# Optimization experiments

Measured on AMD Instinct MI355X. Metric: run time of the kernel, lower is better.

## Reference

```python
import jax, jax.numpy as jnp
import numpy as np

T, H, P = 8192, 512, 512
DT_MIN, DT_MAX = 0.001, 0.1
STEP_RESCALE = 1.0


def setup_inputs() -> dict:
    key = jax.random.key(0)
    ks = jax.random.split(key, 8)
    x = jax.random.normal(ks[0], (T, H), dtype=jnp.float32)
    # sparse reset flags (episode boundaries)
    mask = jax.random.bernoulli(ks[1], 0.005, (T,)).astype(jnp.float32)
    carry = jnp.zeros((1, P, 2), dtype=jnp.float32)  # initial complex state as (re, im)
    # HiPPO-DPLR-style eigenvalue init: lambda_k = -0.5 + i*pi*k
    lambda_real = -0.5 * jnp.ones((P,), dtype=jnp.float32)
    lambda_imag = jnp.pi * jnp.arange(P, dtype=jnp.float32)
    b = jax.random.normal(ks[2], (P, H, 2), dtype=jnp.float32) / np.sqrt(H)
    c = jax.random.normal(ks[3], (H, P, 2), dtype=jnp.float32) * np.sqrt(0.5)
    d = jax.random.normal(ks[4], (H,), dtype=jnp.float32)
    u = jax.random.uniform(ks[5], (P, 1), dtype=jnp.float32)
    log_step = np.log(DT_MIN) + u * (np.log(DT_MAX) - np.log(DT_MIN))
    return {"x": x, "mask": mask, "carry": carry, "lambda_real": lambda_real,
            "lambda_imag": lambda_imag, "b": b, "c": c, "d": d, "log_step": log_step}


def _binary_operator_reset(q_i, q_j):
    a_i, b_i, c_i = q_i
    a_j, b_j, c_j = q_j
    a_out = a_j * a_i * (1.0 - c_j) + a_j * c_j
    b_out = (a_j * b_i + b_j) * (1.0 - c_j) + b_j * c_j
    c_out = c_i * (1.0 - c_j) + c_j
    return (a_out, b_out, c_out)


def reference(x, mask, carry, lambda_real, lambda_imag, b, c, d, log_step):
    t = x.shape[0]
    # clip_eigens=True: force stability
    lam_re = jnp.minimum(lambda_real, -0.0001)
    lam = jax.lax.complex(lam_re, lambda_imag).astype(jnp.complex64)  # [P]
    b_tilde = jax.lax.complex(b[..., 0], b[..., 1]).astype(jnp.complex64)  # [P,H]
    c_tilde = jax.lax.complex(c[..., 0], c[..., 1]).astype(jnp.complex64)  # [H,P]
    step = (STEP_RESCALE * jnp.exp(log_step[:, 0].astype(jnp.float32))).astype(jnp.complex64)  # [P]
    # ZOH discretization
    lambda_bar = jnp.exp(lam * step)                      # [P]
    b_bar = ((lambda_bar - 1.0) / lam)[:, None] * b_tilde  # [P,H]
    # scan elements
    a = jnp.broadcast_to(lambda_bar, (t, P))
    a = jnp.concatenate([jnp.ones((1, P), dtype=lambda_bar.dtype), a])  # [T+1,P]
    b_x = x.astype(jnp.complex64) @ b_bar.T                              # [T,P]
    carry0 = jax.lax.complex(carry[..., 0], carry[..., 1]).astype(jnp.complex64)  # [1,P]
    b_x = jnp.concatenate([carry0, b_x])                                 # [T+1,P]
    m = jnp.concatenate([jnp.zeros((1,), x.dtype), mask])[:, None]       # [T+1,1]
    _, states, _ = jax.lax.associative_scan(_binary_operator_reset, (a, b_x, m))
    states = states[1:]                                                  # [T,P] complex
    ys = jnp.real(states @ c_tilde.T) + d * x                            # [T,H]
    final_carry = states[-1][None]                                       # [1,P] complex
    return (final_carry, ys)
```

## Files before the change

### kernel.cpp

```cpp
#include <hip/hip_runtime.h>
#include <hip/hip_bf16.h>

#define T_LEN 8192
#define H_DIM 512
#define P_DIM 512
#define CS 16
#define NB (T_LEN / CS)

typedef __attribute__((ext_vector_type(8))) __bf16 bf16x8;
typedef __attribute__((ext_vector_type(4))) float f32x4;

__device__ __forceinline__ unsigned short f2bf(float f) {
    __bf16 h = (__bf16)f;
    return __builtin_bit_cast(unsigned short, h);
}
__device__ __forceinline__ float bf2f(unsigned short u) {
    unsigned v = ((unsigned)u) << 16;
    return __builtin_bit_cast(float, v);
}

__device__ __forceinline__ void gload_lds16(void* g, void* l) {
    __builtin_amdgcn_global_load_lds(
        (__attribute__((address_space(1))) unsigned*)g,
        (__attribute__((address_space(3))) unsigned*)l, 16, 0, 0);
}

__global__ __launch_bounds__(512) void precompute_p1(
    const float* __restrict__ lambda_real,
    const float* __restrict__ lambda_imag,
    const float* __restrict__ log_step,
    double* __restrict__ lbar,
    double* __restrict__ coef) {
    int p = threadIdx.x;
    double lr = fmin((double)lambda_real[p], -1e-4);
    double li = (double)lambda_imag[p];
    double step = exp((double)log_step[p]);
    double er = exp(lr * step);
    double ang = li * step;
    double lbr = er * cos(ang);
    double lbi = er * sin(ang);
    lbar[2 * p] = lbr;
    lbar[2 * p + 1] = lbi;
    double nr = lbr - 1.0, ni = lbi;
    double den = lr * lr + li * li;
    coef[2 * p]     = (nr * lr + ni * li) / den;
    coef[2 * p + 1] = (ni * lr - nr * li) / den;
}

__global__ __launch_bounds__(256) void prep_kernel(
    const float* __restrict__ x,
    const float* __restrict__ b, const float* __restrict__ c,
    const double* __restrict__ coef,
    unsigned short* __restrict__ xhi, unsigned short* __restrict__ xlo,
    unsigned short* __restrict__ Bt1hi, unsigned short* __restrict__ Bt1lo,
    unsigned short* __restrict__ Bt2hi, unsigned short* __restrict__ Bt2lo) {
    int idx = blockIdx.x * 256 + threadIdx.x;
    {
        float4 v = ((const float4*)x)[idx];
        ushort4 h, l;
        h.x = f2bf(v.x); l.x = f2bf(v.x - bf2f(h.x));
        h.y = f2bf(v.y); l.y = f2bf(v.y - bf2f(h.y));
        h.z = f2bf(v.z); l.z = f2bf(v.z - bf2f(h.z));
        h.w = f2bf(v.w); l.w = f2bf(v.w - bf2f(h.w));
        ((ushort4*)xhi)[idx] = h;
        ((ushort4*)xlo)[idx] = l;
    }
    if (blockIdx.x < (P_DIM * H_DIM) / 256) {
        int idx2 = blockIdx.x * 256 + threadIdx.x;
        {
            int p = idx2 >> 9, h = idx2 & 511;
            double cr = coef[2 * p], ci = coef[2 * p + 1];
            float2 bv = ((const float2*)b)[(size_t)p * H_DIM + h];
            float re = (float)(cr * (double)bv.x - ci * (double)bv.y);
            float im = (float)(cr * (double)bv.y + ci * (double)bv.x);
            unsigned short rh = f2bf(re), ih = f2bf(im);
            Bt1hi[(size_t)(2 * p) * H_DIM + h]     = rh;
            Bt1lo[(size_t)(2 * p) * H_DIM + h]     = f2bf(re - bf2f(rh));
            Bt1hi[(size_t)(2 * p + 1) * H_DIM + h] = ih;
            Bt1lo[(size_t)(2 * p + 1) * H_DIM + h] = f2bf(im - bf2f(ih));
        }
        {
            int h = idx2 >> 9, p = idx2 & 511;
            float2 cv = ((const float2*)c)[(size_t)h * P_DIM + p];
            float re = cv.x, im = -cv.y;
            ushort2 hi, lo;
            hi.x = f2bf(re); lo.x = f2bf(re - bf2f(hi.x));
            hi.y = f2bf(im); lo.y = f2bf(im - bf2f(hi.y));
            ((ushort2*)Bt2hi)[(size_t)h * P_DIM + p] = hi;
            ((ushort2*)Bt2lo)[(size_t)h * P_DIM + p] = lo;
        }
    }
}

template <int MODE>
__global__ __launch_bounds__(256) void gemm_mfma_split(
    const unsigned short* __restrict__ Ahi, const unsigned short* __restrict__ Alo,
    int lda,
    const unsigned short* __restrict__ Bthi, const unsigned short* __restrict__ Btlo,
    int ldb,
    void* __restrict__ Cout0, void* __restrict__ Cout1, int ldc, int K,
    const float* __restrict__ Dvec, const float* __restrict__ X,
    const float* __restrict__ mask, const double* __restrict__ lbar,
    double* __restrict__ cA, double* __restrict__ cS, float* __restrict__ cC) {
    __shared__ __align__(16) unsigned short lds[2][4][128 * 32];
    const int tid = threadIdx.x;
    const int lane = tid & 63, wid = tid >> 6;
    const int wm = wid >> 1, wn = wid & 1;

    const int id = blockIdx.y * gridDim.x + blockIdx.x;
    const int nx = gridDim.x, rpx = gridDim.y >> 3;
    const int xcd = id & 7, j = id >> 3;
    const int by = xcd * rpx + j / nx;
    const int bx = j % nx;
    const int bm = by * 128, bn = bx * 128;

    const unsigned short* ssrc;
    int srow0, sld;
    if (wid == 0)      { ssrc = Ahi;  srow0 = bm; sld = lda; }
    else if (wid == 1) { ssrc = Alo;  srow0 = bm; sld = lda; }
    else if (wid == 2) { ssrc = Bthi; srow0 = bn; sld = ldb; }
    else               { ssrc = Btlo; srow0 = bn; sld = ldb; }

    f32x4 acc[4][4];
#pragma unroll
    for (int i = 0; i < 4; ++i)
#pragma unroll
        for (int j2 = 0; j2 < 4; ++j2) acc[i][j2] = (f32x4)(0.0f);

    auto stage = [&](int buf, int k0) {
        unsigned short* base = &lds[buf][wid][0];
#pragma unroll
        for (int s = 0; s < 8; ++s) {
            int r = s * 16 + (lane >> 2);
            int cg = (lane & 3) ^ ((r >> 1) & 3);
            void* g = (void*)((const char*)(ssrc + (size_t)(srow0 + r) * sld + k0)
                              + cg * 16);
            gload_lds16(g, (void*)((char*)base + s * 1024));
        }
    };

    stage(0, 0);
    __syncthreads();

    const int nk = K / 32;
    for (int t = 0; t < nk; ++t) {
        int cur = t & 1;
        if (t + 1 < nk) stage(cur ^ 1, (t + 1) * 32);

        bf16x8 ah[4], al[4], bh[4], bl[4];
#pragma unroll
        for (int i = 0; i < 4; ++i) {
            int rA = wm * 64 + i * 16 + (lane & 15);
            int byA = rA * 64 + ((((lane >> 4)) ^ ((rA >> 1) & 3)) << 4);
            ah[i] = *(const bf16x8*)((const char*)&lds[cur][0][0] + byA);
            al[i] = *(const bf16x8*)((const char*)&lds[cur][1][0] + byA);
            int rB = wn * 64 + i * 16 + (lane & 15);
            int byB = rB * 64 + ((((lane >> 4)) ^ ((rB >> 1) & 3)) << 4);
            bh[i] = *(const bf16x8*)((const char*)&lds[cur][2][0] + byB);
            bl[i] = *(const bf16x8*)((const char*)&lds[cur][3][0] + byB);
        }
#pragma unroll
        for (int i = 0; i < 4; ++i)
#pragma unroll
            for (int j2 = 0; j2 < 4; ++j2) {
                acc[i][j2] = __builtin_amdgcn_mfma_f32_16x16x32_bf16(
                    ah[i], bh[j2], acc[i][j2], 0, 0, 0);
                acc[i][j2] = __builtin_amdgcn_mfma_f32_16x16x32_bf16(
                    ah[i], bl[j2], acc[i][j2], 0, 0, 0);
                acc[i][j2] = __builtin_amdgcn_mfma_f32_16x16x32_bf16(
                    al[i], bh[j2], acc[i][j2], 0, 0, 0);
            }
        __syncthreads();
    }

#pragma unroll
    for (int i = 0; i < 4; ++i)
#pragma unroll
        for (int j2 = 0; j2 < 4; ++j2) {
            int col = bn + wn * 64 + j2 * 16 + (lane & 15);
#pragma unroll
            for (int r = 0; r < 4; ++r) {
                int row = bm + wm * 64 + i * 16 + (lane >> 4) * 4 + r;
                float v = acc[i][j2][r];
                if (MODE == 0) {
                    unsigned short h = f2bf(v);
                    unsigned short lo = f2bf(v - bf2f(h));
                    ((unsigned short*)Cout0)[(size_t)row * ldc + col] = h;
                    ((unsigned short*)Cout1)[(size_t)row * ldc + col] = lo;
                } else {
                    v += Dvec[col] * X[(size_t)row * ldc + col];
                    ((float*)Cout0)[(size_t)row * ldc + col] = v;
                }
            }
        }

    if constexpr (MODE == 0) {
        float* fl = (float*)&lds[0][0][0];
#pragma unroll
        for (int i = 0; i < 4; ++i)
#pragma unroll
            for (int j2 = 0; j2 < 4; ++j2) {
                int lcol = wn * 64 + j2 * 16 + (lane & 15);
#pragma unroll
                for (int r = 0; r < 4; ++r) {
                    int lrow = wm * 64 + i * 16 + (lane >> 4) * 4 + r;
                    fl[lrow * 128 + lcol] = acc[i][j2][r];
                }
            }
        __syncthreads();
        const int NCH = 128 / CS;
        for (int w = tid; w < 64 * NCH; w += 256) {
            int q = w & 63;
            int ck = w >> 6;
            int pg = (bn >> 1) + q;
            double lbr = lbar[2 * pg], lbi = lbar[2 * pg + 1];
            double Ar = 1., Ai = 0., Sr = 0., Si = 0.;
            float Cc = 0.f;
            for (int k = 0; k < CS; ++k) {
                int row = ck * CS + k;
                float m = mask[bm + row];
                double bxr = (double)fl[row * 128 + 2 * q];
                double bxi = (double)fl[row * 128 + 2 * q + 1];
                if (m != 0.f) {
                    Ar = lbr; Ai = lbi; Sr = bxr; Si = bxi; Cc = 1.f;
                } else {
                    double nAr = lbr * Ar - lbi * Ai;
                    Ai = lbr * Ai + lbi * Ar; Ar = nAr;
                    double nSr = lbr * Sr - lbi * Si + bxr;
                    Si = lbr * Si + lbi * Sr + bxi; Sr = nSr;
                }
            }
            int cg = (bm / CS) + ck;
            cA[(size_t)cg * 1024 + 2 * pg]     = Ar;
            cA[(size_t)cg * 1024 + 2 * pg + 1] = Ai;
            cS[(size_t)cg * 1024 + 2 * pg]     = Sr;
            cS[(size_t)cg * 1024 + 2 * pg + 1] = Si;
            cC[(size_t)cg * P_DIM + pg] = Cc;
        }
    }
}

__global__ __launch_bounds__(NB) void scanB_kernel(
    const double* __restrict__ cA, const double* __restrict__ cS,
    const float* __restrict__ cC, const float* __restrict__ carry,
    double* __restrict__ prefix) {
    int p = blockIdx.x;
    int i = threadIdx.x;
    __shared__ double sAr[NB], sAi[NB], sSr[NB], sSi[NB];
    __shared__ float sC[NB];

    double Ar = cA[(size_t)i * 1024 + 2 * p];
    double Ai = cA[(size_t)i * 1024 + 2 * p + 1];
    double Sr = cS[(size_t)i * 1024 + 2 * p];
    double Si = cS[(size_t)i * 1024 + 2 * p + 1];
    float  C  = cC[(size_t)i * P_DIM + p];
    sAr[i] = Ar; sAi[i] = Ai; sSr[i] = Sr; sSi[i] = Si; sC[i] = C;
    __syncthreads();

    for (int step = 1; step < NB; step <<= 1) {
        double pAr = 0, pAi = 0, pSr = 0, pSi = 0; float pC = 0;
        if (i >= step) {
            pAr = sAr[i - step]; pAi = sAi[i - step];
            pSr = sSr[i - step]; pSi = sSi[i - step]; pC = sC[i - step];
        }
        __syncthreads();
        if (i >= step && C == 0.f) {
            double nAr = Ar * pAr - Ai * pAi;
            double nAi = Ar * pAi + Ai * pAr;
            double nSr = Ar * pSr - Ai * pSi + Sr;
            double nSi = Ar * pSi + Ai * pSr + Si;
            Ar = nAr; Ai = nAi; Sr = nSr; Si = nSi; C = pC;
        }
        sAr[i] = Ar; sAi[i] = Ai; sSr[i] = Sr; sSi[i] = Si; sC[i] = C;
        __syncthreads();
    }

    double c0r = (double)carry[2 * p], c0i = (double)carry[2 * p + 1];
    double pr, pi_;
    if (i == 0) {
        pr = c0r; pi_ = c0i;
    } else {
        double Lr = sAr[i - 1], Li = sAi[i - 1];
        double Tr = sSr[i - 1], Ti = sSi[i - 1];
        float  LC = sC[i - 1];
        if (LC != 0.f) { pr = Tr; pi_ = Ti; }
        else {
            pr  = Lr * c0r - Li * c0i + Tr;
            pi_ = Lr * c0i + Li * c0r + Ti;
        }
    }
    prefix[(size_t)i * 1024 + 2 * p]     = pr;
    prefix[(size_t)i * 1024 + 2 * p + 1] = pi_;
}

__global__ __launch_bounds__(512) void scanC_kernel(
    unsigned short* __restrict__ Shi, unsigned short* __restrict__ Slo,
    const float* __restrict__ mask, const double* __restrict__ lbar,
    const double* __restrict__ prefix,
    float* __restrict__ carry_out, int carry_elems) {
    int p = threadIdx.x;
    int blk = blockIdx.x;
    double lbr = lbar[2 * p], lbi = lbar[2 * p + 1];
    double sr = prefix[(size_t)blk * 1024 + 2 * p];
    double si = prefix[(size_t)blk * 1024 + 2 * p + 1];
    ushort2* H2 = (ushort2*)Shi;
    ushort2* L2 = (ushort2*)Slo;
    int t0 = blk * CS;
    for (int t = t0; t < t0 + CS; ++t) {
        float m = mask[t];
        ushort2 h2 = H2[(size_t)t * P_DIM + p];
        ushort2 l2 = L2[(size_t)t * P_DIM + p];
        double bxr = (double)(bf2f(h2.x) + bf2f(l2.x));
        double bxi = (double)(bf2f(h2.y) + bf2f(l2.y));
        if (m != 0.f) {
            sr = bxr; si = bxi;
        } else {
            double nr = lbr * sr - lbi * si + bxr;
            si = lbr * si + lbi * sr + bxi;
            sr = nr;
        }
        float sf = (float)sr, sif = (float)si;
        ushort2 ho, lo;
        ho.x = f2bf(sf);  lo.x = f2bf(sf - bf2f(ho.x));
        ho.y = f2bf(sif); lo.y = f2bf(sif - bf2f(ho.y));
        H2[(size_t)t * P_DIM + p] = ho;
        L2[(size_t)t * P_DIM + p] = lo;
    }
    if (blk == NB - 1) {
        if (carry_elems >= 1024) {
            carry_out[2 * p] = (float)sr;
            carry_out[2 * p + 1] = (float)si;
        } else {
            carry_out[p] = (float)sr;
        }
    }
}

extern "C" void kernel_launch(void* const* d_in, const int* in_sizes, int n_in,
                              void* d_out, int out_size, void* d_ws, size_t ws_size,
                              hipStream_t stream) {
    const float* x           = (const float*)d_in[0];
    const float* mask        = (const float*)d_in[1];
    const float* carry       = (const float*)d_in[2];
    const float* lambda_real = (const float*)d_in[3];
    const float* lambda_imag = (const float*)d_in[4];
    const float* b           = (const float*)d_in[5];
    const float* c           = (const float*)d_in[6];
    const float* d           = (const float*)d_in[7];
    const float* log_step    = (const float*)d_in[8];

    float* out = (float*)d_out;
    char* ws = (char*)d_ws;

    int carry_elems = out_size - T_LEN * H_DIM;
    if (carry_elems != 512 && carry_elems != 1024) carry_elems = 1024;
    float* ys_out = out + carry_elems;

    double* lbar   = (double*)ws;                        ws += 1024 * 8;
    double* coef   = (double*)ws;                        ws += 1024 * 8;
    double* cA     = (double*)ws;                        ws += (size_t)NB * 1024 * 8;
    double* cSb    = (double*)ws;                        ws += (size_t)NB * 1024 * 8;
    double* prefix = (double*)ws;                        ws += (size_t)NB * 1024 * 8;
    float* cC      = (float*)ws;                         ws += (size_t)NB * P_DIM * 4;
    unsigned short* xhi   = (unsigned short*)ws;         ws += (size_t)T_LEN * H_DIM * 2;
    unsigned short* xlo   = (unsigned short*)ws;         ws += (size_t)T_LEN * H_DIM * 2;
    unsigned short* Bt1hi = (unsigned short*)ws;         ws += (size_t)(2 * P_DIM) * H_DIM * 2;
    unsigned short* Bt1lo = (unsigned short*)ws;         ws += (size_t)(2 * P_DIM) * H_DIM * 2;
    unsigned short* Bt2hi = (unsigned short*)ws;         ws += (size_t)H_DIM * (2 * P_DIM) * 2;
    unsigned short* Bt2lo = (unsigned short*)ws;         ws += (size_t)H_DIM * (2 * P_DIM) * 2;
    unsigned short* Shi   = (unsigned short*)ws;         ws += (size_t)T_LEN * (2 * P_DIM) * 2;
    unsigned short* Slo   = (unsigned short*)ws;         ws += (size_t)T_LEN * (2 * P_DIM) * 2;

    precompute_p1<<<1, 512, 0, stream>>>(lambda_real, lambda_imag, log_step,
                                         lbar, coef);
    prep_kernel<<<(T_LEN * H_DIM / 4) / 256, 256, 0, stream>>>(
        x, b, c, coef, xhi, xlo, Bt1hi, Bt1lo, Bt2hi, Bt2lo);

    {
        dim3 grid((2 * P_DIM) / 128, T_LEN / 128);
        gemm_mfma_split<0><<<grid, 256, 0, stream>>>(
            xhi, xlo, H_DIM, Bt1hi, Bt1lo, H_DIM,
            Shi, Slo, 2 * P_DIM, H_DIM, nullptr, nullptr,
            mask, lbar, cA, cSb, cC);
    }

    scanB_kernel<<<P_DIM, NB, 0, stream>>>(cA, cSb, cC, carry, prefix);
    scanC_kernel<<<NB, 512, 0, stream>>>(Shi, Slo, mask, lbar, prefix, out,
                                         carry_elems);

    {
        dim3 grid(H_DIM / 128, T_LEN / 128);
        gemm_mfma_split<1><<<grid, 256, 0, stream>>>(
            Shi, Slo, 2 * P_DIM, Bt2hi, Bt2lo, 2 * P_DIM,
            ys_out, nullptr, H_DIM, 2 * P_DIM, d, x,
            nullptr, nullptr, nullptr, nullptr, nullptr);
    }
}
```

Before: 111.3 us.

## Drop precompute kernel by recomputing discretization inline; use wave-shuffle scan in scanB

```diff
diff --git a/kernel.cpp b/kernel.cpp
--- a/kernel.cpp
+++ b/kernel.cpp
@@ -25,32 +25,23 @@
         (__attribute__((address_space(3))) unsigned*)l, 16, 0, 0);
 }
 
-__global__ __launch_bounds__(512) void precompute_p1(
-    const float* __restrict__ lambda_real,
-    const float* __restrict__ lambda_imag,
-    const float* __restrict__ log_step,
-    double* __restrict__ lbar,
-    double* __restrict__ coef) {
-    int p = threadIdx.x;
-    double lr = fmin((double)lambda_real[p], -1e-4);
-    double li = (double)lambda_imag[p];
+__device__ __forceinline__ void lbar_of(const float* lam_re, const float* lam_im,
+                                        const float* log_step, int p,
+                                        double& lbr, double& lbi) {
+    double lr = fmin((double)lam_re[p], -1e-4);
+    double li = (double)lam_im[p];
     double step = exp((double)log_step[p]);
     double er = exp(lr * step);
     double ang = li * step;
-    double lbr = er * cos(ang);
-    double lbi = er * sin(ang);
-    lbar[2 * p] = lbr;
-    lbar[2 * p + 1] = lbi;
-    double nr = lbr - 1.0, ni = lbi;
-    double den = lr * lr + li * li;
-    coef[2 * p]     = (nr * lr + ni * li) / den;
-    coef[2 * p + 1] = (ni * lr - nr * li) / den;
+    lbr = er * cos(ang);
+    lbi = er * sin(ang);
 }
 
 __global__ __launch_bounds__(256) void prep_kernel(
     const float* __restrict__ x,
     const float* __restrict__ b, const float* __restrict__ c,
-    const double* __restrict__ coef,
+    const float* __restrict__ lam_re, const float* __restrict__ lam_im,
+    const float* __restrict__ log_step,
     unsigned short* __restrict__ xhi, unsigned short* __restrict__ xlo,
     unsigned short* __restrict__ Bt1hi, unsigned short* __restrict__ Bt1lo,
     unsigned short* __restrict__ Bt2hi, unsigned short* __restrict__ Bt2lo) {
@@ -69,7 +60,16 @@
         int idx2 = blockIdx.x * 256 + threadIdx.x;
         {
             int p = idx2 >> 9, h = idx2 & 511;
-            double cr = coef[2 * p], ci = coef[2 * p + 1];
+            double lr = fmin((double)lam_re[p], -1e-4);
+            double li = (double)lam_im[p];
+            double step = exp((double)log_step[p]);
+            double er = exp(lr * step);
+            double ang = li * step;
+            double lbr = er * cos(ang), lbi = er * sin(ang);
+            double nr = lbr - 1.0, ni = lbi;
+            double den = lr * lr + li * li;
+            double cr = (nr * lr + ni * li) / den;
+            double ci = (ni * lr - nr * li) / den;
             float2 bv = ((const float2*)b)[(size_t)p * H_DIM + h];
             float re = (float)(cr * (double)bv.x - ci * (double)bv.y);
             float im = (float)(cr * (double)bv.y + ci * (double)bv.x);
@@ -100,7 +100,9 @@
     int ldb,
     void* __restrict__ Cout0, void* __restrict__ Cout1, int ldc, int K,
     const float* __restrict__ Dvec, const float* __restrict__ X,
-    const float* __restrict__ mask, const double* __restrict__ lbar,
+    const float* __restrict__ mask,
+    const float* __restrict__ lam_re, const float* __restrict__ lam_im,
+    const float* __restrict__ log_step,
     double* __restrict__ cA, double* __restrict__ cS, float* __restrict__ cC) {
     __shared__ __align__(16) unsigned short lds[2][4][128 * 32];
     const int tid = threadIdx.x;
@@ -209,11 +211,12 @@
             }
         __syncthreads();
         const int NCH = 128 / CS;
+        int q = tid & 63;
+        int pg = (bn >> 1) + q;
+        double lbr, lbi;
+        lbar_of(lam_re, lam_im, log_step, pg, lbr, lbi);
         for (int w = tid; w < 64 * NCH; w += 256) {
-            int q = w & 63;
             int ck = w >> 6;
-            int pg = (bn >> 1) + q;
-            double lbr = lbar[2 * pg], lbi = lbar[2 * pg + 1];
             double Ar = 1., Ai = 0., Sr = 0., Si = 0.;
             float Cc = 0.f;
             for (int k = 0; k < CS; ++k) {
@@ -246,48 +249,73 @@
     double* __restrict__ prefix) {
     int p = blockIdx.x;
     int i = threadIdx.x;
-    __shared__ double sAr[NB], sAi[NB], sSr[NB], sSi[NB];
-    __shared__ float sC[NB];
+    int lane = i & 63, w = i >> 6;
+    __shared__ double tAr[8], tAi[8], tSr[8], tSi[8];
+    __shared__ float  tC[8];
+    __shared__ double eAr[8], eAi[8], eSr[8], eSi[8];
+    __shared__ float  eC[8];
 
     double Ar = cA[(size_t)i * 1024 + 2 * p];
     double Ai = cA[(size_t)i * 1024 + 2 * p + 1];
     double Sr = cS[(size_t)i * 1024 + 2 * p];
     double Si = cS[(size_t)i * 1024 + 2 * p + 1];
     float  C  = cC[(size_t)i * P_DIM + p];
-    sAr[i] = Ar; sAi[i] = Ai; sSr[i] = Sr; sSi[i] = Si; sC[i] = C;
-    __syncthreads();
-
-    for (int step = 1; step < NB; step <<= 1) {
-        double pAr = 0, pAi = 0, pSr = 0, pSi = 0; float pC = 0;
-        if (i >= step) {
-            pAr = sAr[i - step]; pAi = sAi[i - step];
-            pSr = sSr[i - step]; pSi = sSi[i - step]; pC = sC[i - step];
-        }
-        __syncthreads();
-        if (i >= step && C == 0.f) {
+
+#pragma unroll
+    for (int d = 1; d < 64; d <<= 1) {
+        double pAr = __shfl_up(Ar, d), pAi = __shfl_up(Ai, d);
+        double pSr = __shfl_up(Sr, d), pSi = __shfl_up(Si, d);
+        float  pC  = __shfl_up(C, d);
+        if (lane >= d && C == 0.f) {
             double nAr = Ar * pAr - Ai * pAi;
             double nAi = Ar * pAi + Ai * pAr;
             double nSr = Ar * pSr - Ai * pSi + Sr;
             double nSi = Ar * pSi + Ai * pSr + Si;
             Ar = nAr; Ai = nAi; Sr = nSr; Si = nSi; C = pC;
         }
-        sAr[i] = Ar; sAi[i] = Ai; sSr[i] = Sr; sSi[i] = Si; sC[i] = C;
-        __syncthreads();
-    }
-
+    }
+    if (lane == 63) { tAr[w] = Ar; tAi[w] = Ai; tSr[w] = Sr; tSi[w] = Si; tC[w] = C; }
+    __syncthreads();
+
+    if (i == 0) {
+        double rAr = 1., rAi = 0., rSr = 0., rSi = 0.; float rC = 0.f;
+        for (int k = 0; k < 8; ++k) {
+            eAr[k] = rAr; eAi[k] = rAi; eSr[k] = rSr; eSi[k] = rSi; eC[k] = rC;
+            double gAr = tAr[k], gAi = tAi[k], gSr = tSr[k], gSi = tSi[k];
+            float gC = tC[k];
+            if (gC != 0.f) { rAr = gAr; rAi = gAi; rSr = gSr; rSi = gSi; rC = gC; }
+            else {
+                double nAr = gAr * rAr - gAi * rAi;
+                double nAi = gAr * rAi + gAi * rAr;
+                double nSr = gAr * rSr - gAi * rSi + gSr;
+                double nSi = gAr * rSi + gAi * rSr + gSi;
+                rAr = nAr; rAi = nAi; rSr = nSr; rSi = nSi;
+            }
+        }
+    }
+    __syncthreads();
+
+    double pAr = __shfl_up(Ar, 1), pAi = __shfl_up(Ai, 1);
+    double pSr = __shfl_up(Sr, 1), pSi = __shfl_up(Si, 1);
+    float  pC  = __shfl_up(C, 1);
+    double fAr, fAi, fSr, fSi; float fC;
+    if (lane == 0) {
+        fAr = eAr[w]; fAi = eAi[w]; fSr = eSr[w]; fSi = eSi[w]; fC = eC[w];
+    } else if (pC != 0.f) {
+        fAr = pAr; fAi = pAi; fSr = pSr; fSi = pSi; fC = pC;
+    } else {
+        fAr = pAr * eAr[w] - pAi * eAi[w];
+        fAi = pAr * eAi[w] + pAi * eAr[w];
+        fSr = pAr * eSr[w] - pAi * eSi[w] + pSr;
+        fSi = pAr * eSi[w] + pAi * eSr[w] + pSi;
+        fC = eC[w];
+    }
     double c0r = (double)carry[2 * p], c0i = (double)carry[2 * p + 1];
     double pr, pi_;
-    if (i == 0) {
-        pr = c0r; pi_ = c0i;
-    } else {
-        double Lr = sAr[i - 1], Li = sAi[i - 1];
-        double Tr = sSr[i - 1], Ti = sSi[i - 1];
-        float  LC = sC[i - 1];
-        if (LC != 0.f) { pr = Tr; pi_ = Ti; }
-        else {
-            pr  = Lr * c0r - Li * c0i + Tr;
-            pi_ = Lr * c0i + Li * c0r + Ti;
-        }
+    if (fC != 0.f) { pr = fSr; pi_ = fSi; }
+    else {
+        pr  = fAr * c0r - fAi * c0i + fSr;
+        pi_ = fAr * c0i + fAi * c0r + fSi;
     }
     prefix[(size_t)i * 1024 + 2 * p]     = pr;
     prefix[(size_t)i * 1024 + 2 * p + 1] = pi_;
@@ -295,12 +323,15 @@
 
 __global__ __launch_bounds__(512) void scanC_kernel(
     unsigned short* __restrict__ Shi, unsigned short* __restrict__ Slo,
-    const float* __restrict__ mask, const double* __restrict__ lbar,
+    const float* __restrict__ mask,
+    const float* __restrict__ lam_re, const float* __restrict__ lam_im,
+    const float* __restrict__ log_step,
     const double* __restrict__ prefix,
     float* __restrict__ carry_out, int carry_elems) {
     int p = threadIdx.x;
     int blk = blockIdx.x;
-    double lbr = lbar[2 * p], lbi = lbar[2 * p + 1];
+    double lbr, lbi;
+    lbar_of(lam_re, lam_im, log_step, p, lbr, lbi);
     double sr = prefix[(size_t)blk * 1024 + 2 * p];
     double si = prefix[(size_t)blk * 1024 + 2 * p + 1];
     ushort2* H2 = (ushort2*)Shi;
@@ -356,8 +387,6 @@
     if (carry_elems != 512 && carry_elems != 1024) carry_elems = 1024;
     float* ys_out = out + carry_elems;
 
-    double* lbar   = (double*)ws;                        ws += 1024 * 8;
-    double* coef   = (double*)ws;                        ws += 1024 * 8;
     double* cA     = (double*)ws;                        ws += (size_t)NB * 1024 * 8;
     double* cSb    = (double*)ws;                        ws += (size_t)NB * 1024 * 8;
     double* prefix = (double*)ws;                        ws += (size_t)NB * 1024 * 8;
@@ -371,28 +400,28 @@
     unsigned short* Shi   = (unsigned short*)ws;         ws += (size_t)T_LEN * (2 * P_DIM) * 2;
     unsigned short* Slo   = (unsigned short*)ws;         ws += (size_t)T_LEN * (2 * P_DIM) * 2;
 
-    precompute_p1<<<1, 512, 0, stream>>>(lambda_real, lambda_imag, log_step,
-                                         lbar, coef);
     prep_kernel<<<(T_LEN * H_DIM / 4) / 256, 256, 0, stream>>>(
-        x, b, c, coef, xhi, xlo, Bt1hi, Bt1lo, Bt2hi, Bt2lo);
+        x, b, c, lambda_real, lambda_imag, log_step,
+        xhi, xlo, Bt1hi, Bt1lo, Bt2hi, Bt2lo);
 
     {
         dim3 grid((2 * P_DIM) / 128, T_LEN / 128);
         gemm_mfma_split<0><<<grid, 256, 0, stream>>>(
             xhi, xlo, H_DIM, Bt1hi, Bt1lo, H_DIM,
             Shi, Slo, 2 * P_DIM, H_DIM, nullptr, nullptr,
-            mask, lbar, cA, cSb, cC);
+            mask, lambda_real, lambda_imag, log_step, cA, cSb, cC);
     }
 
     scanB_kernel<<<P_DIM, NB, 0, stream>>>(cA, cSb, cC, carry, prefix);
-    scanC_kernel<<<NB, 512, 0, stream>>>(Shi, Slo, mask, lbar, prefix, out,
-                                         carry_elems);
+    scanC_kernel<<<NB, 512, 0, stream>>>(Shi, Slo, mask,
+                                         lambda_real, lambda_imag, log_step,
+                                         prefix, out, carry_elems);
 
     {
         dim3 grid(H_DIM / 128, T_LEN / 128);
         gemm_mfma_split<1><<<grid, 256, 0, stream>>>(
             Shi, Slo, 2 * P_DIM, Bt2hi, Bt2lo, 2 * P_DIM,
             ys_out, nullptr, H_DIM, 2 * P_DIM, d, x,
-            nullptr, nullptr, nullptr, nullptr, nullptr);
-    }
-}
+            nullptr, nullptr, nullptr, nullptr, nullptr, nullptr, nullptr);
+    }
+}
```

Result: faster. 107.9 us (median of 2 runs) (-3.1%).
